# Performance work log

Hardware: AMD Instinct MI355X
Metric: run time of the kernel (lower is better)

## Reference

```python
import jax, jax.numpy as jnp
import numpy as np
from jax import lax

PAD_TOKEN = 1
VOCAB = 32000
HID = 512
B, T, M = 32, 512, 6


def setup_inputs() -> dict:
    key = jax.random.key(0)
    ks = jax.random.split(key, 12)
    lim_g = 1.0 / np.sqrt(HID)
    lim_w = 1.0 / np.sqrt(2 * HID)
    u = lambda k, shape, lim: jax.random.uniform(k, shape, jnp.float32, -lim, lim)
    inp = {
        "input_seqs": jax.random.randint(ks[0], (B, T, M), 0, VOCAB, dtype=jnp.int32),
        "input_lengths": jax.random.randint(ks[1], (B,), 1, T + 1, dtype=jnp.int32),
        "emb": jax.random.normal(ks[2], (VOCAB, HID), jnp.float32),
        # forward GRU cell (Keras GRUCell, reset_after=True)
        "k_f": u(ks[3], (HID, 3 * HID), lim_g),
        "rk_f": u(ks[4], (HID, 3 * HID), lim_g),
        "b_f": u(ks[5], (2, 3 * HID), lim_g),
        # backward GRU cell
        "k_b": u(ks[6], (HID, 3 * HID), lim_g),
        "rk_b": u(ks[7], (HID, 3 * HID), lim_g),
        "b_b": u(ks[8], (2, 3 * HID), lim_g),
        # output projection W: 2H -> H
        "Wk": u(ks[9], (2 * HID, HID), lim_w),
        "Wb": u(ks[10], (HID,), lim_w),
    }
    return inp


def _gru_dir(x, mask, kernel, rkernel, bias, reverse):
    """Masked GRU scan. x: [B,T,H], mask: [B,T] bool. Keras GRUCell (reset_after=True).
    Masked timesteps carry previous state/output through (Keras semantics)."""
    b_in, b_rec = bias[0], bias[1]
    xs = x @ kernel + b_in                      # [B,T,3H], precompute input GEMM
    xs_t = jnp.swapaxes(xs, 0, 1)               # [T,B,3H]
    m_t = jnp.swapaxes(mask, 0, 1)              # [T,B]
    h0 = jnp.zeros((x.shape[0], rkernel.shape[0]), x.dtype)

    def step(h, inp):
        xt, mt = inp
        inner = h @ rkernel + b_rec             # [B,3H]
        xz, xr, xh = jnp.split(xt, 3, axis=-1)
        iz, ir, ih = jnp.split(inner, 3, axis=-1)
        z = jax.nn.sigmoid(xz + iz)
        r = jax.nn.sigmoid(xr + ir)
        hh = jnp.tanh(xh + r * ih)
        hn = z * h + (1.0 - z) * hh
        hn = jnp.where(mt[:, None], hn, h)      # masked step: carry state
        return hn, hn

    hT, outs = lax.scan(step, h0, (xs_t, m_t), reverse=reverse)
    return jnp.swapaxes(outs, 0, 1), hT         # [B,T,H], [B,H]


def reference(input_seqs, input_lengths, emb, k_f, rk_f, b_f, k_b, rk_b, b_b, Wk, Wb):
    # embedding lookup + PAD masking, sum over memory-tuple axis
    e = emb[input_seqs]                                       # [B,T,M,H]
    pad_mask = (input_seqs != PAD_TOKEN).astype(e.dtype)      # [B,T,M]
    embedded = jnp.sum(e * pad_mask[..., None], axis=2)       # [B,T,H]
    # (dropout p=0.0 -> identity)

    time_mask = jnp.arange(T)[None, :] < input_lengths[:, None]  # [B,T] bool

    out_f, h_f = _gru_dir(embedded, time_mask, k_f, rk_f, b_f, reverse=False)
    out_b, h_b = _gru_dir(embedded, time_mask, k_b, rk_b, b_b, reverse=True)

    outputs = jnp.concatenate([out_f, out_b], axis=-1)        # [B,T,2H]
    hidden_hat = jnp.concatenate([h_f, h_b], axis=-1)         # [B,2H]

    hidden = hidden_hat @ Wk + Wb                             # [B,H]
    outputs = outputs @ Wk + Wb                               # [B,T,H]
    return outputs, hidden
```

## Files before the change

### kernel.cpp

```cpp
#include <hip/hip_runtime.h>

typedef _Float16 f16;
typedef f16  f16x8 __attribute__((ext_vector_type(8)));
typedef float f32x4 __attribute__((ext_vector_type(4)));
typedef unsigned int u32;
typedef unsigned long long u64;
typedef u32 u32x4 __attribute__((ext_vector_type(4)));

#define NB   32
#define NT   512
#define NM   6
#define NH   512
#define NH3  1536
#define PADTOK 1
#define LO_SCALE 4096.0f
#define LO_INV   (1.0f/4096.0f)

#define FLAGS_OFF 168165376
#define SLOT_STRIDE 544
#define FLAGS_U32 (2 * 32 * SLOT_STRIDE)

__global__ __launch_bounds__(128) void k_embed(const int* __restrict__ seqs,
                                               const float* __restrict__ emb,
                                               f16* __restrict__ Ahi,
                                               f16* __restrict__ Alo,
                                               f16* __restrict__ A2,
                                               u32* __restrict__ flags) {
  int row = blockIdx.x;
  int tid = threadIdx.x;
  if (row < 32) {
    for (int c2 = tid; c2 < 1024; c2 += 128)
      A2[(size_t)(16416 + row) * 1024 + c2] = (f16)0.f;
  }
  if (row < 64) {
    for (int j = row * 128 + tid; j < FLAGS_U32; j += 64 * 128)
      flags[j] = 0u;
  }
  const int* tr = seqs + (size_t)row * NM;
  int c0 = tid * 4;
  float acc0 = 0.f, acc1 = 0.f, acc2 = 0.f, acc3 = 0.f;
  for (int m = 0; m < NM; m++) {
    int tk = tr[m];
    if (tk != PADTOK) {
      float4 ev = *(const float4*)(emb + (size_t)tk * NH + c0);
      acc0 += ev.x; acc1 += ev.y; acc2 += ev.z; acc3 += ev.w;
    }
  }
  float a[4] = {acc0, acc1, acc2, acc3};
  for (int j = 0; j < 4; j++) {
    float v = a[j];
    f16 h = (f16)v;
    float lo = (v - (float)h) * LO_SCALE;
    Ahi[(size_t)row * NH + c0 + j] = h;
    Alo[(size_t)row * NH + c0 + j] = (f16)lo;
  }
}

__global__ __launch_bounds__(256) void k_gemm_in(const f16* __restrict__ Ahi,
                                                 const f16* __restrict__ Alo,
                                                 const float* __restrict__ Bw,
                                                 const float* __restrict__ bias,
                                                 f16* __restrict__ Cxs,
                                                 f16* __restrict__ Clo) {
  __shared__ f16 BsH[64][40];
  __shared__ f16 BsL[64][40];
  int bx = blockIdx.x, by = blockIdx.y;
  int tid = threadIdx.x;
  int w = tid >> 6, l = tid & 63;
  int row0 = bx * 64 + w * 16;
  int col0 = by * 64;
  int arow = row0 + (l & 15);
  int kg = (l >> 4) * 8;
  f32x4 acc[4], accs[4];
  for (int nt = 0; nt < 4; nt++) {
    float bv = bias[col0 + nt * 16 + (l & 15)];
    f32x4 t = {bv, bv, bv, bv};
    acc[nt] = t;
    f32x4 z = {0.f, 0.f, 0.f, 0.f};
    accs[nt] = z;
  }
  for (int kb = 0; kb < NH; kb += 32) {
    __syncthreads();
    for (int idx = tid; idx < 2048; idx += 256) {
      int n = idx & 63, kl = idx >> 6;
      float v = Bw[(size_t)(kb + kl) * NH3 + col0 + n];
      f16 h = (f16)v;
      BsH[n][kl] = h;
      BsL[n][kl] = (f16)((v - (float)h) * LO_SCALE);
    }
    __syncthreads();
    f16x8 ah = *(const f16x8*)(Ahi + (size_t)arow * NH + kb + kg);
    f16x8 al = *(const f16x8*)(Alo + (size_t)arow * NH + kb + kg);
    for (int nt = 0; nt < 4; nt++) {
      f16x8 bh = *(const f16x8*)(&BsH[nt * 16 + (l & 15)][kg]);
      f16x8 bl = *(const f16x8*)(&BsL[nt * 16 + (l & 15)][kg]);
      acc[nt]  = __builtin_amdgcn_mfma_f32_16x16x32_f16(ah, bh, acc[nt], 0, 0, 0);
      accs[nt] = __builtin_amdgcn_mfma_f32_16x16x32_f16(al, bh, accs[nt], 0, 0, 0);
      accs[nt] = __builtin_amdgcn_mfma_f32_16x16x32_f16(ah, bl, accs[nt], 0, 0, 0);
    }
  }
  for (int nt = 0; nt < 4; nt++)
    for (int r = 0; r < 4; r++) {
      int grow = row0 + (l >> 4) * 4 + r;
      int gcol = col0 + nt * 16 + (l & 15);
      int pr = (grow & (NT - 1)) * 32 + (grow >> 9);
      float v = acc[nt][r] + accs[nt][r] * LO_INV;
      f16 h = (f16)v;
      Cxs[(size_t)pr * NH3 + gcol] = h;
      if (gcol >= 2 * NH)
        Clo[(size_t)pr * NH + (gcol - 2 * NH)] = (f16)(v - (float)h);
    }
}

__global__ __launch_bounds__(128) void k_recur(const f16* __restrict__ xs_f,
                                               const f16* __restrict__ xs_b,
                                               const f16* __restrict__ xhlo_f,
                                               const f16* __restrict__ xhlo_b,
                                               const float* __restrict__ rk_f,
                                               const float* __restrict__ rk_b,
                                               const float* __restrict__ b_f,
                                               const float* __restrict__ b_b,
                                               const int* __restrict__ lens,
                                               u32* __restrict__ hb32,
                                               f16* __restrict__ A2,
                                               u32* __restrict__ flags) {
  __shared__ f16 WsH[48 * 512];
  __shared__ f16 WsL[48 * 512];
  int wg = blockIdx.x;
  int d = wg >> 5;
  int s = wg & 31;
  int u0 = s * 16;
  int tid = threadIdx.x;
  int w = tid >> 6, l = tid & 63;
  const f16*   xs = d ? xs_b : xs_f;
  const f16*   xlo = d ? xhlo_b : xhlo_f;
  const float* rk = d ? rk_b : rk_f;
  const float* bb = d ? b_b  : b_f;

  for (int idx = tid; idx < 48 * 512; idx += 128) {
    int k = idx / 48, n = idx % 48;
    int gcol = (n >> 4) * NH + u0 + (n & 15);
    float v = rk[(size_t)k * NH3 + gcol];
    f16 h = (f16)v;
    f16 lo = (f16)((v - (float)h) * LO_SCALE);
    int byte = (n * 1024 + k * 2) ^ ((n & 7) << 4);
    *(f16*)((char*)WsH + byte) = h;
    *(f16*)((char*)WsL + byte) = lo;
  }
  __syncthreads();

  int c = l & 15;
  float brz = bb[NH3 + 0 * NH + u0 + c];
  float brr = bb[NH3 + 1 * NH + u0 + c];
  float brh = bb[NH3 + 2 * NH + u0 + c];
  int mrow[4], lenv[4];
  float hstate[4];
  int wi_h[4];
  for (int r = 0; r < 4; r++) {
    int b = w * 16 + (l >> 4) * 4 + r;
    mrow[r] = b;
    lenv[r] = lens[b];
    hstate[r] = 0.f;
    wi_h[r] = b * NH + u0 + c;
  }
  const int PLANE = NB * NH;
  const int fbase = (d * 32 + s) * SLOT_STRIDE;
  for (int r = 0; r < 4; r++)
    __hip_atomic_store(&hb32[(d * 2 + 0) * PLANE + wi_h[r]], 0u,
                       __ATOMIC_RELAXED, __HIP_MEMORY_SCOPE_AGENT);
  asm volatile("s_waitcnt vmcnt(0)" ::: "memory");
  __syncthreads();
  if (tid == 0)
    __hip_atomic_store(&flags[fbase + 0], 1u,
                       __ATOMIC_RELAXED, __HIP_MEMORY_SCOPE_AGENT);

  int arow_b = w * 16 + (l & 15);
  int kg = (l >> 4) * 8;
  int cbase = c * 1024;
  int zc = (c & 7) << 4;

#pragma unroll 1
  for (int i = 0; i < NT; i++) {
    int t = d ? (NT - 1 - i) : i;
    int p = i & 1;
    const u32* hrow = hb32 + (size_t)(d * 2 + p) * PLANE + arow_b * NH;
    u32* wplane = hb32 + (size_t)(d * 2 + (p ^ 1)) * PLANE;
    const unsigned short* xrow = (const unsigned short*)(xs + (size_t)t * 32 * NH3);
    const unsigned short* xlorow = (const unsigned short*)(xlo + (size_t)t * 32 * NH);

    if (tid < 32) {
      const u32* fp = flags + (d * 32 + tid) * SLOT_STRIDE + i;
      while (__hip_atomic_load(fp, __ATOMIC_RELAXED, __HIP_MEMORY_SCOPE_AGENT) == 0u)
        __builtin_amdgcn_s_sleep(1);
    }
    __syncthreads();

    u64 q[16][4];
#pragma unroll
    for (int kk = 0; kk < 16; kk++) {
      const u32* fb = hrow + kk * 32 + kg;
#pragma unroll
      for (int j = 0; j < 4; j++)
        q[kk][j] = __hip_atomic_load((const u64*)(fb + 2 * j),
                                     __ATOMIC_RELAXED, __HIP_MEMORY_SCOPE_AGENT);
    }
    unsigned short rxz[4], rxr[4], rxh[4], rxl[4];
#pragma unroll
    for (int r = 0; r < 4; r++) {
      size_t o = (size_t)mrow[r] * NH3 + u0 + c;
      rxz[r] = xrow[o];
      rxr[r] = xrow[o + NH];
      rxh[r] = xrow[o + 2 * NH];
      rxl[r] = xlorow[(size_t)mrow[r] * NH + u0 + c];
    }

    f32x4 a0, a1, a2, s0, s1, s2;
#pragma unroll
    for (int r = 0; r < 4; r++) {
      a0[r] = 0.f; a1[r] = 0.f; a2[r] = 0.f;
      s0[r] = 0.f; s1[r] = 0.f; s2[r] = 0.f;
    }
#pragma unroll
    for (int kk = 0; kk < 16; kk++) {
      union { u32x4 w; f16x8 h; } A, L;
#pragma unroll
      for (int j = 0; j < 4; j++) {
        u32 w0 = (u32)q[kk][j];
        u32 w1 = (u32)(q[kk][j] >> 32);
        A.w[j] = __builtin_amdgcn_perm(w1, w0, 0x05040100u);
        L.w[j] = __builtin_amdgcn_perm(w1, w0, 0x07060302u);
      }
      int kb2 = (kk * 32 + kg) * 2;
      int off = (cbase + kb2) ^ zc;
      f16x8 b0h = *(const f16x8*)((const char*)WsH + off);
      f16x8 b1h = *(const f16x8*)((const char*)WsH + 16384 + off);
      f16x8 b2h = *(const f16x8*)((const char*)WsH + 32768 + off);
      f16x8 b0l = *(const f16x8*)((const char*)WsL + off);
      f16x8 b1l = *(const f16x8*)((const char*)WsL + 16384 + off);
      f16x8 b2l = *(const f16x8*)((const char*)WsL + 32768 + off);
      a0 = __builtin_amdgcn_mfma_f32_16x16x32_f16(A.h, b0h, a0, 0, 0, 0);
      s0 = __builtin_amdgcn_mfma_f32_16x16x32_f16(L.h, b0h, s0, 0, 0, 0);
      s0 = __builtin_amdgcn_mfma_f32_16x16x32_f16(A.h, b0l, s0, 0, 0, 0);
      a1 = __builtin_amdgcn_mfma_f32_16x16x32_f16(A.h, b1h, a1, 0, 0, 0);
      s1 = __builtin_amdgcn_mfma_f32_16x16x32_f16(L.h, b1h, s1, 0, 0, 0);
      s1 = __builtin_amdgcn_mfma_f32_16x16x32_f16(A.h, b1l, s1, 0, 0, 0);
      a2 = __builtin_amdgcn_mfma_f32_16x16x32_f16(A.h, b2h, a2, 0, 0, 0);
      s2 = __builtin_amdgcn_mfma_f32_16x16x32_f16(L.h, b2h, s2, 0, 0, 0);
      s2 = __builtin_amdgcn_mfma_f32_16x16x32_f16(A.h, b2l, s2, 0, 0, 0);
    }

#pragma unroll
    for (int r = 0; r < 4; r++) {
      union { unsigned short u; f16 f; } uz, ur, uh, ul;
      uz.u = rxz[r]; ur.u = rxr[r]; uh.u = rxh[r]; ul.u = rxl[r];
      float az = a0[r] + s0[r] * LO_INV + (float)uz.f + brz;
      float ar = a1[r] + s1[r] * LO_INV + (float)ur.f + brr;
      float ahg = a2[r] + s2[r] * LO_INV;
      float xh = (float)uh.f + (float)ul.f;
      float z  = 1.f / (1.f + __expf(-az));
      float rr = 1.f / (1.f + __expf(-ar));
      float hh = tanhf(xh + rr * (ahg + brh));
      float hn = z * hstate[r] + (1.f - z) * hh;
      bool msk = t < lenv[r];
      hn = msk ? hn : hstate[r];
      hstate[r] = hn;
      union { f16 f; unsigned short u; } chv, clv;
      chv.f = (f16)hn;
      float lof = (hn - (float)chv.f) * LO_SCALE;
      clv.f = (f16)lof;
      u32 packed = (u32)chv.u | ((u32)clv.u << 16);
      __hip_atomic_store(&wplane[wi_h[r]], packed,
                         __ATOMIC_RELAXED, __HIP_MEMORY_SCOPE_AGENT);
    }
    asm volatile("s_waitcnt vmcnt(0)" ::: "memory");
    __syncthreads();
    if (tid == 0)
      __hip_atomic_store(&flags[fbase + i + 1], 1u,
                         __ATOMIC_RELAXED, __HIP_MEMORY_SCOPE_AGENT);
#pragma unroll
    for (int r = 0; r < 4; r++)
      A2[((size_t)mrow[r] * NT + t) * 1024 + d * NH + u0 + c] = (f16)hstate[r];
  }
  for (int r = 0; r < 4; r++)
    A2[(size_t)(16384 + mrow[r]) * 1024 + d * NH + u0 + c] = (f16)hstate[r];
}

__global__ __launch_bounds__(256) void k_gemm_out(const f16* __restrict__ A2,
                                                  const float* __restrict__ Wk,
                                                  const float* __restrict__ Wb,
                                                  float* __restrict__ Out) {
  __shared__ f16 Bs[64][40];
  int bx = blockIdx.x, by = blockIdx.y;
  int tid = threadIdx.x;
  int w = tid >> 6, l = tid & 63;
  int row0 = bx * 64 + w * 16;
  int col0 = by * 64;
  int arow = row0 + (l & 15);
  int kg = (l >> 4) * 8;
  f32x4 acc[4];
  for (int nt = 0; nt < 4; nt++) {
    float bv = Wb[col0 + nt * 16 + (l & 15)];
    f32x4 t = {bv, bv, bv, bv};
    acc[nt] = t;
  }
  for (int kb = 0; kb < 1024; kb += 32) {
    __syncthreads();
    for (int idx = tid; idx < 2048; idx += 256) {
      int n = idx & 63, kl = idx >> 6;
      Bs[n][kl] = (f16)Wk[(size_t)(kb + kl) * NH + col0 + n];
    }
    __syncthreads();
    f16x8 av = *(const f16x8*)(A2 + (size_t)arow * 1024 + kb + kg);
    for (int nt = 0; nt < 4; nt++) {
      f16x8 bv = *(const f16x8*)(&Bs[nt * 16 + (l & 15)][kg]);
      acc[nt] = __builtin_amdgcn_mfma_f32_16x16x32_f16(av, bv, acc[nt], 0, 0, 0);
    }
  }
  for (int nt = 0; nt < 4; nt++)
    for (int r = 0; r < 4; r++) {
      int grow = row0 + (l >> 4) * 4 + r;
      if (grow < 16416)
        Out[(size_t)grow * NH + col0 + nt * 16 + (l & 15)] = acc[nt][r];
    }
}

extern "C" void kernel_launch(void* const* d_in, const int* in_sizes, int n_in,
                              void* d_out, int out_size, void* d_ws, size_t ws_size,
                              hipStream_t stream) {
  (void)in_sizes; (void)n_in; (void)out_size; (void)ws_size;
  const int*   seqs = (const int*)d_in[0];
  const int*   lens = (const int*)d_in[1];
  const float* emb  = (const float*)d_in[2];
  const float* k_f  = (const float*)d_in[3];
  const float* rk_f = (const float*)d_in[4];
  const float* b_f  = (const float*)d_in[5];
  const float* k_b  = (const float*)d_in[6];
  const float* rk_b = (const float*)d_in[7];
  const float* b_b  = (const float*)d_in[8];
  const float* Wk   = (const float*)d_in[9];
  const float* Wb   = (const float*)d_in[10];
  float* out = (float*)d_out;
  char* ws = (char*)d_ws;
  f16* A2     = (f16*)(ws + 0);
  f16* Ahi    = (f16*)(ws + 0);
  f16* Alo    = (f16*)(ws + 16777216);
  f16* xs_f   = (f16*)(ws + 33685504);
  f16* xs_b   = (f16*)(ws + 84017152);
  f16* xhlo_f = (f16*)(ws + 134348800);
  f16* xhlo_b = (f16*)(ws + 151126016);
  u32* hb32   = (u32*)(ws + 167903232);
  u32* flags  = (u32*)(ws + FLAGS_OFF);

  hipLaunchKernelGGL(k_embed, dim3(16384), dim3(128), 0, stream, seqs, emb, Ahi, Alo, A2, flags);
  hipLaunchKernelGGL(k_gemm_in, dim3(256, 24), dim3(256), 0, stream, Ahi, Alo, k_f, b_f, xs_f, xhlo_f);
  hipLaunchKernelGGL(k_gemm_in, dim3(256, 24), dim3(256), 0, stream, Ahi, Alo, k_b, b_b, xs_b, xhlo_b);
  hipLaunchKernelGGL(k_recur, dim3(64), dim3(128), 0, stream,
                     xs_f, xs_b, xhlo_f, xhlo_b, rk_f, rk_b, b_f, b_b, lens, hb32, A2, flags);
  hipLaunchKernelGGL(k_gemm_out, dim3(257, 8), dim3(256), 0, stream, A2, Wk, Wb, out);
}
```

Baseline: 4.569 ms.

## Drop hidden-state lo split, use ring-buffered f16 h exchange and tiled xs layout

The hidden state exchanged between workgroups becomes a single f16 value instead of a packed hi/lo pair. It is written with coherent short stores into a ring of planes (512 or 64 deep, depending on workspace size) instead of a ping-pong double buffer, and read with plain vector loads. This removes the 64-bit atomic loads, the permutes and one third of the recurrent MFMAs. The input-projection output is rearranged per timestep and per slice so each step reads one contiguous tile. The cost is lower precision of the recurrent h operand, which may drift over 512 steps, and ring reuse could race when the ring is small.

```diff
diff --git a/kernel.cpp b/kernel.cpp
--- a/kernel.cpp
+++ b/kernel.cpp
@@ -4,8 +4,7 @@
 typedef f16  f16x8 __attribute__((ext_vector_type(8)));
 typedef float f32x4 __attribute__((ext_vector_type(4)));
 typedef unsigned int u32;
-typedef unsigned long long u64;
-typedef u32 u32x4 __attribute__((ext_vector_type(4)));
+typedef unsigned short u16;
 
 #define NB   32
 #define NT   512
@@ -16,9 +15,17 @@
 #define LO_SCALE 4096.0f
 #define LO_INV   (1.0f/4096.0f)
 
-#define FLAGS_OFF 168165376
+#define XS2F_OFF  33685504
+#define XS2B_OFF  100794368
+#define HB_OFF    167903232
 #define SLOT_STRIDE 544
 #define FLAGS_U32 (2 * 32 * SLOT_STRIDE)
+#define PLANE_E   16384
+
+__device__ __forceinline__ void coh_store_u16(u16* base, u32 voff, u32 val) {
+  asm volatile("global_store_short %0, %1, %2 sc0 sc1"
+               :: "v"(voff), "v"(val), "s"(base) : "memory");
+}
 
 __global__ __launch_bounds__(128) void k_embed(const int* __restrict__ seqs,
                                                const float* __restrict__ emb,
@@ -60,8 +67,7 @@
                                                  const f16* __restrict__ Alo,
                                                  const float* __restrict__ Bw,
                                                  const float* __restrict__ bias,
-                                                 f16* __restrict__ Cxs,
-                                                 f16* __restrict__ Clo) {
+                                                 f16* __restrict__ xs2) {
   __shared__ f16 BsH[64][40];
   __shared__ f16 BsL[64][40];
   int bx = blockIdx.x, by = blockIdx.y;
@@ -102,28 +108,31 @@
   for (int nt = 0; nt < 4; nt++)
     for (int r = 0; r < 4; r++) {
       int grow = row0 + (l >> 4) * 4 + r;
+      int b = grow >> 9, t = grow & (NT - 1);
       int gcol = col0 + nt * 16 + (l & 15);
-      int pr = (grow & (NT - 1)) * 32 + (grow >> 9);
+      int g = gcol >> 9, u = gcol & 511;
+      int ss = u >> 4, cc = u & 15;
       float v = acc[nt][r] + accs[nt][r] * LO_INV;
       f16 h = (f16)v;
-      Cxs[(size_t)pr * NH3 + gcol] = h;
-      if (gcol >= 2 * NH)
-        Clo[(size_t)pr * NH + (gcol - 2 * NH)] = (f16)(v - (float)h);
-    }
-}
-
-__global__ __launch_bounds__(128) void k_recur(const f16* __restrict__ xs_f,
-                                               const f16* __restrict__ xs_b,
-                                               const f16* __restrict__ xhlo_f,
-                                               const f16* __restrict__ xhlo_b,
+      size_t idx = (size_t)(t * 32 + ss) * 2048 + g * 512 + b * 16 + cc;
+      xs2[idx] = h;
+      if (g == 2)
+        xs2[idx + 512] = (f16)(v - (float)h);
+    }
+}
+
+__global__ __launch_bounds__(128) void k_recur(const f16* __restrict__ xs2_f,
+                                               const f16* __restrict__ xs2_b,
                                                const float* __restrict__ rk_f,
                                                const float* __restrict__ rk_b,
                                                const float* __restrict__ b_f,
                                                const float* __restrict__ b_b,
                                                const int* __restrict__ lens,
-                                               u32* __restrict__ hb32,
+                                               u16* __restrict__ hb_f,
+                                               u16* __restrict__ hb_b,
                                                f16* __restrict__ A2,
-                                               u32* __restrict__ flags) {
+                                               u32* __restrict__ flags,
+                                               int ring_mask) {
   __shared__ f16 WsH[48 * 512];
   __shared__ f16 WsL[48 * 512];
   int wg = blockIdx.x;
@@ -132,8 +141,8 @@
   int u0 = s * 16;
   int tid = threadIdx.x;
   int w = tid >> 6, l = tid & 63;
-  const f16*   xs = d ? xs_b : xs_f;
-  const f16*   xlo = d ? xhlo_b : xhlo_f;
+  const f16*   xs2 = d ? xs2_b : xs2_f;
+  u16*         myhb = d ? hb_b : hb_f;
   const float* rk = d ? rk_b : rk_f;
   const float* bb = d ? b_b  : b_f;
 
@@ -155,19 +164,17 @@
   float brh = bb[NH3 + 2 * NH + u0 + c];
   int mrow[4], lenv[4];
   float hstate[4];
-  int wi_h[4];
+  u32 vo_h[4];
   for (int r = 0; r < 4; r++) {
     int b = w * 16 + (l >> 4) * 4 + r;
     mrow[r] = b;
     lenv[r] = lens[b];
     hstate[r] = 0.f;
-    wi_h[r] = b * NH + u0 + c;
-  }
-  const int PLANE = NB * NH;
+    vo_h[r] = (u32)(s * 1024 + b * 32 + c * 2);
+  }
   const int fbase = (d * 32 + s) * SLOT_STRIDE;
   for (int r = 0; r < 4; r++)
-    __hip_atomic_store(&hb32[(d * 2 + 0) * PLANE + wi_h[r]], 0u,
-                       __ATOMIC_RELAXED, __HIP_MEMORY_SCOPE_AGENT);
+    coh_store_u16(myhb, vo_h[r], 0u);
   asm volatile("s_waitcnt vmcnt(0)" ::: "memory");
   __syncthreads();
   if (tid == 0)
@@ -178,15 +185,13 @@
   int kg = (l >> 4) * 8;
   int cbase = c * 1024;
   int zc = (c & 7) << 4;
+  int hbase_lane = (kg >> 4) * 1024 + arow_b * 32 + (kg & 15) * 2;
 
 #pragma unroll 1
   for (int i = 0; i < NT; i++) {
     int t = d ? (NT - 1 - i) : i;
-    int p = i & 1;
-    const u32* hrow = hb32 + (size_t)(d * 2 + p) * PLANE + arow_b * NH;
-    u32* wplane = hb32 + (size_t)(d * 2 + (p ^ 1)) * PLANE;
-    const unsigned short* xrow = (const unsigned short*)(xs + (size_t)t * 32 * NH3);
-    const unsigned short* xlorow = (const unsigned short*)(xlo + (size_t)t * 32 * NH);
+    const u16* hplane = myhb + (size_t)(i & ring_mask) * PLANE_E;
+    u16* wplane = myhb + (size_t)((i + 1) & ring_mask) * PLANE_E;
 
     if (tid < 32) {
       const u32* fp = flags + (d * 32 + tid) * SLOT_STRIDE + i;
@@ -195,23 +200,15 @@
     }
     __syncthreads();
 
-    u64 q[16][4];
-#pragma unroll
-    for (int kk = 0; kk < 16; kk++) {
-      const u32* fb = hrow + kk * 32 + kg;
-#pragma unroll
-      for (int j = 0; j < 4; j++)
-        q[kk][j] = __hip_atomic_load((const u64*)(fb + 2 * j),
-                                     __ATOMIC_RELAXED, __HIP_MEMORY_SCOPE_AGENT);
-    }
-    unsigned short rxz[4], rxr[4], rxh[4], rxl[4];
-#pragma unroll
-    for (int r = 0; r < 4; r++) {
-      size_t o = (size_t)mrow[r] * NH3 + u0 + c;
-      rxz[r] = xrow[o];
-      rxr[r] = xrow[o + NH];
-      rxh[r] = xrow[o + 2 * NH];
-      rxl[r] = xlorow[(size_t)mrow[r] * NH + u0 + c];
+    const u16* sl = (const u16*)(xs2 + (size_t)(t * 32 + s) * 2048);
+    u16 rxz[4], rxr[4], rxh[4], rxl[4];
+#pragma unroll
+    for (int r = 0; r < 4; r++) {
+      int bo = mrow[r] * 16 + c;
+      rxz[r] = sl[bo];
+      rxr[r] = sl[512 + bo];
+      rxh[r] = sl[1024 + bo];
+      rxl[r] = sl[1536 + bo];
     }
 
     f32x4 a0, a1, a2, s0, s1, s2;
@@ -222,14 +219,7 @@
     }
 #pragma unroll
     for (int kk = 0; kk < 16; kk++) {
-      union { u32x4 w; f16x8 h; } A, L;
-#pragma unroll
-      for (int j = 0; j < 4; j++) {
-        u32 w0 = (u32)q[kk][j];
-        u32 w1 = (u32)(q[kk][j] >> 32);
-        A.w[j] = __builtin_amdgcn_perm(w1, w0, 0x05040100u);
-        L.w[j] = __builtin_amdgcn_perm(w1, w0, 0x07060302u);
-      }
+      f16x8 ah = *(const f16x8*)((const char*)hplane + hbase_lane + kk * 2048);
       int kb2 = (kk * 32 + kg) * 2;
       int off = (cbase + kb2) ^ zc;
       f16x8 b0h = *(const f16x8*)((const char*)WsH + off);
@@ -238,20 +228,17 @@
       f16x8 b0l = *(const f16x8*)((const char*)WsL + off);
       f16x8 b1l = *(const f16x8*)((const char*)WsL + 16384 + off);
       f16x8 b2l = *(const f16x8*)((const char*)WsL + 32768 + off);
-      a0 = __builtin_amdgcn_mfma_f32_16x16x32_f16(A.h, b0h, a0, 0, 0, 0);
-      s0 = __builtin_amdgcn_mfma_f32_16x16x32_f16(L.h, b0h, s0, 0, 0, 0);
-      s0 = __builtin_amdgcn_mfma_f32_16x16x32_f16(A.h, b0l, s0, 0, 0, 0);
-      a1 = __builtin_amdgcn_mfma_f32_16x16x32_f16(A.h, b1h, a1, 0, 0, 0);
-      s1 = __builtin_amdgcn_mfma_f32_16x16x32_f16(L.h, b1h, s1, 0, 0, 0);
-      s1 = __builtin_amdgcn_mfma_f32_16x16x32_f16(A.h, b1l, s1, 0, 0, 0);
-      a2 = __builtin_amdgcn_mfma_f32_16x16x32_f16(A.h, b2h, a2, 0, 0, 0);
-      s2 = __builtin_amdgcn_mfma_f32_16x16x32_f16(L.h, b2h, s2, 0, 0, 0);
-      s2 = __builtin_amdgcn_mfma_f32_16x16x32_f16(A.h, b2l, s2, 0, 0, 0);
-    }
-
-#pragma unroll
-    for (int r = 0; r < 4; r++) {
-      union { unsigned short u; f16 f; } uz, ur, uh, ul;
+      a0 = __builtin_amdgcn_mfma_f32_16x16x32_f16(ah, b0h, a0, 0, 0, 0);
+      s0 = __builtin_amdgcn_mfma_f32_16x16x32_f16(ah, b0l, s0, 0, 0, 0);
+      a1 = __builtin_amdgcn_mfma_f32_16x16x32_f16(ah, b1h, a1, 0, 0, 0);
+      s1 = __builtin_amdgcn_mfma_f32_16x16x32_f16(ah, b1l, s1, 0, 0, 0);
+      a2 = __builtin_amdgcn_mfma_f32_16x16x32_f16(ah, b2h, a2, 0, 0, 0);
+      s2 = __builtin_amdgcn_mfma_f32_16x16x32_f16(ah, b2l, s2, 0, 0, 0);
+    }
+
+#pragma unroll
+    for (int r = 0; r < 4; r++) {
+      union { u16 u; f16 f; } uz, ur, uh, ul;
       uz.u = rxz[r]; ur.u = rxr[r]; uh.u = rxh[r]; ul.u = rxl[r];
       float az = a0[r] + s0[r] * LO_INV + (float)uz.f + brz;
       float ar = a1[r] + s1[r] * LO_INV + (float)ur.f + brr;
@@ -264,13 +251,9 @@
       bool msk = t < lenv[r];
       hn = msk ? hn : hstate[r];
       hstate[r] = hn;
-      union { f16 f; unsigned short u; } chv, clv;
+      union { f16 f; u16 u; } chv;
       chv.f = (f16)hn;
-      float lof = (hn - (float)chv.f) * LO_SCALE;
-      clv.f = (f16)lof;
-      u32 packed = (u32)chv.u | ((u32)clv.u << 16);
-      __hip_atomic_store(&wplane[wi_h[r]], packed,
-                         __ATOMIC_RELAXED, __HIP_MEMORY_SCOPE_AGENT);
+      coh_store_u16(wplane, vo_h[r], (u32)chv.u);
     }
     asm volatile("s_waitcnt vmcnt(0)" ::: "memory");
     __syncthreads();
@@ -327,7 +310,7 @@
 extern "C" void kernel_launch(void* const* d_in, const int* in_sizes, int n_in,
                               void* d_out, int out_size, void* d_ws, size_t ws_size,
                               hipStream_t stream) {
-  (void)in_sizes; (void)n_in; (void)out_size; (void)ws_size;
+  (void)in_sizes; (void)n_in; (void)out_size;
   const int*   seqs = (const int*)d_in[0];
   const int*   lens = (const int*)d_in[1];
   const float* emb  = (const float*)d_in[2];
@@ -344,17 +327,21 @@
   f16* A2     = (f16*)(ws + 0);
   f16* Ahi    = (f16*)(ws + 0);
   f16* Alo    = (f16*)(ws + 16777216);
-  f16* xs_f   = (f16*)(ws + 33685504);
-  f16* xs_b   = (f16*)(ws + 84017152);
-  f16* xhlo_f = (f16*)(ws + 134348800);
-  f16* xhlo_b = (f16*)(ws + 151126016);
-  u32* hb32   = (u32*)(ws + 167903232);
-  u32* flags  = (u32*)(ws + FLAGS_OFF);
+  f16* xs2_f  = (f16*)(ws + XS2F_OFF);
+  f16* xs2_b  = (f16*)(ws + XS2B_OFF);
+
+  int ring = 512;
+  size_t need512 = (size_t)HB_OFF + 2ull * 512 * 32768 + (size_t)FLAGS_U32 * 4;
+  if (ws_size < need512) ring = 64;
+  u16* hb_f = (u16*)(ws + HB_OFF);
+  u16* hb_b = hb_f + (size_t)ring * PLANE_E;
+  u32* flags = (u32*)(ws + HB_OFF + 2ull * ring * 32768);
+  int ring_mask = ring - 1;
 
   hipLaunchKernelGGL(k_embed, dim3(16384), dim3(128), 0, stream, seqs, emb, Ahi, Alo, A2, flags);
-  hipLaunchKernelGGL(k_gemm_in, dim3(256, 24), dim3(256), 0, stream, Ahi, Alo, k_f, b_f, xs_f, xhlo_f);
-  hipLaunchKernelGGL(k_gemm_in, dim3(256, 24), dim3(256), 0, stream, Ahi, Alo, k_b, b_b, xs_b, xhlo_b);
+  hipLaunchKernelGGL(k_gemm_in, dim3(256, 24), dim3(256), 0, stream, Ahi, Alo, k_f, b_f, xs2_f);
+  hipLaunchKernelGGL(k_gemm_in, dim3(256, 24), dim3(256), 0, stream, Ahi, Alo, k_b, b_b, xs2_b);
   hipLaunchKernelGGL(k_recur, dim3(64), dim3(128), 0, stream,
-                     xs_f, xs_b, xhlo_f, xhlo_b, rk_f, rk_b, b_f, b_b, lens, hb32, A2, flags);
+                     xs2_f, xs2_b, rk_f, rk_b, b_f, b_b, lens, hb_f, hb_b, A2, flags, ring_mask);
   hipLaunchKernelGGL(k_gemm_out, dim3(257, 8), dim3(256), 0, stream, A2, Wk, Wb, out);
 }
```

Result: faster. 3.774 ms (-17.4%).
